# Optimization experiments

Measured on AMD Instinct MI355X. Metric: run time of the kernel, lower is better.

Reference implementation:

```python
import jax, jax.numpy as jnp
import numpy as np

L = 32            # fixed label space replacing torch.unique (labels in [0, L))
DELTA_AGG = 0.5
DELTA_DIS = 1.5
REG_W = 0.001


def safe_norm(sq):
    # sqrt with zero-safe gradient: returns 0 where sq == 0
    safe = jnp.where(sq > 0, sq, 1.0)
    return jnp.where(sq > 0, jnp.sqrt(safe), 0.0)


def _single(emb, instance, kernel, training_mask):
    D = emb.shape[0]
    tm = training_mask > 0.5
    kn = kernel > 0.5
    inst = jnp.where(tm, instance, 0).reshape(-1)          # (N,) masked instance labels
    inst_k = jnp.where(tm & kn, instance, 0).reshape(-1)   # (N,) kernel-region labels
    embf = emb.reshape(D, -1).T                            # (N, D)
    ones = jnp.ones(inst.shape, dtype=jnp.float32)

    # per-label kernel means (emb_mean), label 0 stays zero as in torch
    cnt_k = jax.ops.segment_sum(ones, inst_k, num_segments=L)            # (L,)
    sum_k = jax.ops.segment_sum(embf, inst_k, num_segments=L)            # (L, D)
    emb_mean = sum_k / jnp.maximum(cnt_k, 1.0)[:, None]
    emb_mean = emb_mean.at[0].set(0.0)

    present = cnt_k > 0
    num_instance = jnp.sum(present.astype(jnp.int32))
    nz = present & (jnp.arange(L) > 0)

    # aggregation loss: per-pixel distance to own instance's kernel mean
    diff = embf - emb_mean[inst]                                          # (N, D)
    dist = safe_norm(jnp.sum(diff * diff, axis=1))
    val = jnp.log(jax.nn.relu(dist - DELTA_AGG) ** 2 + 1.0)
    sum_v = jax.ops.segment_sum(val, inst, num_segments=L)
    cnt = jax.ops.segment_sum(ones, inst, num_segments=L)
    l_agg_per = sum_v / jnp.maximum(cnt, 1.0)
    l_agg = jnp.sum(jnp.where(nz, l_agg_per, 0.0)) / jnp.maximum(num_instance - 1, 1)

    # discrimination loss: all pairs of distinct non-background present labels
    pdiff = emb_mean[:, None, :] - emb_mean[None, :, :]                   # (L, L, D)
    pdist = safe_norm(jnp.sum(pdiff * pdiff, axis=-1))
    pval = jnp.log(jax.nn.relu(2.0 * DELTA_DIS - pdist) ** 2 + 1.0)
    pmask = nz[:, None] & nz[None, :] & ~jnp.eye(L, dtype=bool)
    n_pairs = jnp.sum(pmask.astype(jnp.float32))
    l_dis = jnp.sum(jnp.where(pmask, pval, 0.0)) / jnp.maximum(n_pairs, 1.0)
    l_dis = jnp.where(num_instance > 2, l_dis, 0.0)

    # regularizer over the num_instance present columns of emb_mean
    reg = jnp.log(safe_norm(jnp.sum(emb_mean * emb_mean, axis=1)) + 1.0)
    l_reg = jnp.sum(jnp.where(present, reg, 0.0)) / jnp.maximum(num_instance, 1) * REG_W

    loss = l_agg + l_dis + l_reg
    return jnp.where(num_instance <= 1, 0.0, loss)


def setup_inputs() -> dict:
    key = jax.random.key(0)
    k1, k2, k3, k4 = jax.random.split(key, 4)
    B, D, H, W = 8, 4, 736, 736
    emb = jax.random.normal(k1, (B, D, H, W), dtype=jnp.float32)
    instance = jax.random.randint(k2, (B, H, W), 0, L, dtype=jnp.int32)
    kernel = jax.random.uniform(k3, (B, H, W), dtype=jnp.float32)
    training_mask = jax.random.uniform(k4, (B, H, W), dtype=jnp.float32)
    return {"emb": emb, "instance": instance, "kernel": kernel, "training_mask": training_mask}


def reference(emb, instance, kernel, training_mask):
    return jax.vmap(_single)(emb, instance, kernel, training_mask)
```

## Files before the change

kernel.cpp:

```cpp
#include <hip/hip_runtime.h>

#define LBL 32
#define NPIX (736 * 736)
#define NQ (NPIX / 4)
#define NB 529
#define BATCH 8
#define DELTA_AGG 0.5f
#define DELTA_DIS 1.5f
#define REG_W 0.001f

#define CE_BASE 0
#define LAB_BASE (BATCH * NPIX * 2)
#define PA_BASE (LAB_BASE + BATCH * NPIX / 4)
#define RED_BASE (PA_BASE + BATCH * 192 * NB)
#define PC_BASE (RED_BASE + BATCH * 256)

__device__ __forceinline__ unsigned short f2bf(float f) {
  unsigned int u = __float_as_uint(f);
  unsigned int r = u + 0x7FFFu + ((u >> 16) & 1u);
  return (unsigned short)(r >> 16);
}
__device__ __forceinline__ float bfl(unsigned int w) {
  return __uint_as_float(w << 16);
}
__device__ __forceinline__ float bfh(unsigned int w) {
  return __uint_as_float(w & 0xFFFF0000u);
}

__global__ __launch_bounds__(256) void kA(
    const float* __restrict__ emb, const int* __restrict__ inst,
    const float* __restrict__ kern, const float* __restrict__ mask,
    float* __restrict__ ws) {
  const int b = blockIdx.y;
  const int t = threadIdx.x;
  __shared__ float s_cnt[LBL];
  __shared__ float s_sum[LBL * 4];
  __shared__ float s_cnta[LBL];
  if (t < LBL) { s_cnt[t] = 0.f; s_cnta[t] = 0.f; }
  if (t < LBL * 4) s_sum[t] = 0.f;
  __syncthreads();

  const long base = (long)b * NPIX;
  const int q = blockIdx.x * 256 + t;
  const int4 iv = ((const int4*)(inst + base))[q];
  const float4 kv = ((const float4*)(kern + base))[q];
  const float4 mv = ((const float4*)(mask + base))[q];
  const float* eb = emb + (long)b * 4 * NPIX;
  const float4 e0 = ((const float4*)(eb))[q];
  const float4 e1 = ((const float4*)(eb + NPIX))[q];
  const float4 e2 = ((const float4*)(eb + 2 * NPIX))[q];
  const float4 e3 = ((const float4*)(eb + 3 * NPIX))[q];

  const int labs[4] = {iv.x, iv.y, iv.z, iv.w};
  const float ks[4] = {kv.x, kv.y, kv.z, kv.w};
  const float ms[4] = {mv.x, mv.y, mv.z, mv.w};
  const float c0[4] = {e0.x, e0.y, e0.z, e0.w};
  const float c1[4] = {e1.x, e1.y, e1.z, e1.w};
  const float c2[4] = {e2.x, e2.y, e2.z, e2.w};
  const float c3[4] = {e3.x, e3.y, e3.z, e3.w};

  bool has0 = false;
  unsigned int labw = 0;
  union { unsigned short us[16]; uint4 v[2]; } pk;
#pragma unroll
  for (int j = 0; j < 4; j++) {
    const bool m = ms[j] > 0.5f;
    const int li = m ? labs[j] : 0;
    const int lk = (m && ks[j] > 0.5f) ? labs[j] : 0;
    labw |= ((unsigned int)li) << (8 * j);
    pk.us[j * 4 + 0] = f2bf(c0[j]);
    pk.us[j * 4 + 1] = f2bf(c1[j]);
    pk.us[j * 4 + 2] = f2bf(c2[j]);
    pk.us[j * 4 + 3] = f2bf(c3[j]);
    if (li > 0) atomicAdd(&s_cnta[li], 1.0f);
    if (lk > 0) {
      atomicAdd(&s_cnt[lk], 1.0f);
      atomicAdd(&s_sum[lk * 4 + 0], c0[j]);
      atomicAdd(&s_sum[lk * 4 + 1], c1[j]);
      atomicAdd(&s_sum[lk * 4 + 2], c2[j]);
      atomicAdd(&s_sum[lk * 4 + 3], c3[j]);
    } else {
      has0 = true;
    }
  }
  const size_t recq = (size_t)b * NQ + q;
  uint4* cep = (uint4*)(ws + CE_BASE);
  cep[recq * 2] = pk.v[0];
  cep[recq * 2 + 1] = pk.v[1];
  ((unsigned int*)(ws + LAB_BASE))[recq] = labw;

  if (has0) s_cnt[0] = 1.0f;
  __syncthreads();
  if (t < 192) {
    const float v = (t < 32) ? s_cnt[t] : (t < 160 ? s_sum[t - 32] : s_cnta[t - 160]);
    ws[PA_BASE + ((size_t)b * 192 + t) * NB + blockIdx.x] = v;
  }
}

__global__ __launch_bounds__(256) void kB(float* __restrict__ ws) {
  const int b = blockIdx.y;
  const int col = blockIdx.x * 4 + (threadIdx.x >> 6);
  const int lane = threadIdx.x & 63;
  const float* p = ws + PA_BASE + ((size_t)b * 192 + col) * NB;
  float s = 0.f;
  for (int g = lane; g < NB; g += 64) s += p[g];
#pragma unroll
  for (int o = 32; o > 0; o >>= 1) s += __shfl_down(s, o);
  if (lane == 0) ws[RED_BASE + b * 256 + col] = s;
}

__global__ __launch_bounds__(256) void kC(float* __restrict__ ws) {
  const int b = blockIdx.y;
  const int t = threadIdx.x;
  __shared__ float s_mean[LBL * 4];
  __shared__ float s_val[LBL];
  const float* rd = ws + RED_BASE + b * 256;
  if (t < LBL * 4) {
    const int l = t >> 2;
    s_mean[t] = (l == 0) ? 0.f : rd[32 + t] / fmaxf(rd[l], 1.0f);
  }
  if (t < LBL) s_val[t] = 0.f;
  __syncthreads();

  const int q = blockIdx.x * 256 + t;
  const size_t recq = (size_t)b * NQ + q;
  const uint4* cep = (const uint4*)(ws + CE_BASE);
  const uint4 r0 = cep[recq * 2];
  const uint4 r1 = cep[recq * 2 + 1];
  const unsigned int labw = ((const unsigned int*)(ws + LAB_BASE))[recq];

  const unsigned int wlo[4] = {r0.x, r0.z, r1.x, r1.z};
  const unsigned int whi[4] = {r0.y, r0.w, r1.y, r1.w};
#pragma unroll
  for (int j = 0; j < 4; j++) {
    const int li = (labw >> (8 * j)) & 0xFF;
    if (li > 0) {
      const float d0 = bfl(wlo[j]) - s_mean[li * 4 + 0];
      const float d1 = bfh(wlo[j]) - s_mean[li * 4 + 1];
      const float d2 = bfl(whi[j]) - s_mean[li * 4 + 2];
      const float d3 = bfh(whi[j]) - s_mean[li * 4 + 3];
      const float sq = d0 * d0 + d1 * d1 + d2 * d2 + d3 * d3;
      const float dist = (sq > 0.f) ? sqrtf(sq) : 0.f;
      const float tt = fmaxf(dist - DELTA_AGG, 0.f);
      atomicAdd(&s_val[li], logf(fmaf(tt, tt, 1.0f)));
    }
  }
  __syncthreads();
  if (t < 32) ws[PC_BASE + ((size_t)b * 32 + t) * NB + blockIdx.x] = s_val[t];
}

__global__ __launch_bounds__(1024) void kD(const float* __restrict__ ws,
                                           float* __restrict__ out) {
  const int b = blockIdx.x;
  const int t = threadIdx.x;
  const int col = t >> 5, sub = t & 31;
  const float* p = ws + PC_BASE + ((size_t)b * 32 + col) * NB;
  float s = 0.f;
  for (int g = sub; g < NB; g += 32) s += p[g];
  __shared__ float red[LBL][33];
  red[col][sub] = s;

  const float* rd = ws + RED_BASE + b * 256;
  __shared__ float sm[LBL * 4];
  __shared__ float scc[LBL];
  __shared__ float sca[LBL];
  if (t >= 512 && t < 640) {
    const int e = t - 512, l = e >> 2;
    sm[e] = (l == 0) ? 0.f : rd[32 + e] / fmaxf(rd[l], 1.0f);
  } else if (t >= 640 && t < 672) {
    scc[t - 640] = rd[t - 640];
  } else if (t >= 672 && t < 704) {
    sca[t - 672] = rd[160 + (t - 672)];
  }
  __syncthreads();
  __shared__ float sv[LBL];
  if (t < 32) {
    float v = 0.f;
#pragma unroll
    for (int k = 0; k < 32; k++) v += red[t][k];
    sv[t] = v;
  }
  __syncthreads();

  if (t < 64) {
    const int lane = t;
    const bool pres = (lane < LBL) && (scc[lane & 31] > 0.f);
    const unsigned long long bal_p = __ballot(pres);
    const int num_instance = __popcll(bal_p);
    const bool nz = pres && (lane > 0);
    const unsigned long long bal_nz = __ballot(nz);

    float agg = 0.f;
    if (nz) agg = sv[lane] / fmaxf(sca[lane], 1.0f);

    float reg = 0.f;
    if (pres) {
      float sq = 0.f;
#pragma unroll
      for (int d = 0; d < 4; d++) sq += sm[lane * 4 + d] * sm[lane * 4 + d];
      const float nrm = (sq > 0.f) ? sqrtf(sq) : 0.f;
      reg = logf(nrm + 1.0f);
    }

    float dis = 0.f, npair = 0.f;
    for (int pi = lane; pi < LBL * LBL; pi += 64) {
      const int i = pi >> 5, j = pi & 31;
      if (i != j && ((bal_nz >> i) & 1ull) && ((bal_nz >> j) & 1ull)) {
        float sq = 0.f;
#pragma unroll
        for (int d = 0; d < 4; d++) {
          const float df = sm[i * 4 + d] - sm[j * 4 + d];
          sq += df * df;
        }
        const float pdist = (sq > 0.f) ? sqrtf(sq) : 0.f;
        const float tt = fmaxf(2.0f * DELTA_DIS - pdist, 0.f);
        dis += logf(fmaf(tt, tt, 1.0f));
        npair += 1.0f;
      }
    }

#pragma unroll
    for (int o = 32; o > 0; o >>= 1) {
      agg += __shfl_down(agg, o);
      reg += __shfl_down(reg, o);
      dis += __shfl_down(dis, o);
      npair += __shfl_down(npair, o);
    }

    if (lane == 0) {
      const float l_agg = agg / fmaxf((float)(num_instance - 1), 1.0f);
      const float l_dis = (num_instance > 2) ? dis / fmaxf(npair, 1.0f) : 0.f;
      const float l_reg = reg / fmaxf((float)num_instance, 1.0f) * REG_W;
      const float loss = l_agg + l_dis + l_reg;
      out[b] = (num_instance <= 1) ? 0.f : loss;
    }
  }
}

extern "C" void kernel_launch(void* const* d_in, const int* in_sizes, int n_in,
                              void* d_out, int out_size, void* d_ws,
                              size_t ws_size, hipStream_t stream) {
  const float* emb = (const float*)d_in[0];
  const int* instance = (const int*)d_in[1];
  const float* kern = (const float*)d_in[2];
  const float* mask = (const float*)d_in[3];
  float* out = (float*)d_out;
  float* ws = (float*)d_ws;

  dim3 gridA(NB, BATCH);
  kA<<<gridA, 256, 0, stream>>>(emb, instance, kern, mask, ws);
  dim3 gridB(48, BATCH);
  kB<<<gridB, 256, 0, stream>>>(ws);
  kC<<<gridA, 256, 0, stream>>>(ws);
  kD<<<BATCH, 1024, 0, stream>>>(ws, out);
}
```

Measured before the change: 185.1 us.

## Re-read fp32 embeddings in second pass instead of stashing bf16 copies

The first pass no longer writes a bf16 copy of the embeddings. The second pass re-reads the original fp32 embeddings, leaving only the packed label word as intermediate state, and the masked-pixel count moves from the first pass to the second. Each thread now handles two quads, which halves the grid. Per-block partials are stored block-major so their writes are contiguous, and the reduction kernels are adjusted to match. This trades the bf16 write and read for a larger fp32 re-read that may be served from cache, and it removes the bf16 rounding error.

```diff
diff --git a/kernel.cpp b/kernel.cpp
--- a/kernel.cpp
+++ b/kernel.cpp
@@ -3,29 +3,17 @@
 #define LBL 32
 #define NPIX (736 * 736)
 #define NQ (NPIX / 4)
-#define NB 529
+#define QPB 512
+#define NBA 265
 #define BATCH 8
 #define DELTA_AGG 0.5f
 #define DELTA_DIS 1.5f
 #define REG_W 0.001f
 
-#define CE_BASE 0
-#define LAB_BASE (BATCH * NPIX * 2)
-#define PA_BASE (LAB_BASE + BATCH * NPIX / 4)
-#define RED_BASE (PA_BASE + BATCH * 192 * NB)
+#define LAB_BASE 0
+#define PA_BASE (BATCH * NQ)
+#define RED_BASE (PA_BASE + BATCH * NBA * 160)
 #define PC_BASE (RED_BASE + BATCH * 256)
-
-__device__ __forceinline__ unsigned short f2bf(float f) {
-  unsigned int u = __float_as_uint(f);
-  unsigned int r = u + 0x7FFFu + ((u >> 16) & 1u);
-  return (unsigned short)(r >> 16);
-}
-__device__ __forceinline__ float bfl(unsigned int w) {
-  return __uint_as_float(w << 16);
-}
-__device__ __forceinline__ float bfh(unsigned int w) {
-  return __uint_as_float(w & 0xFFFF0000u);
-}
 
 __global__ __launch_bounds__(256) void kA(
     const float* __restrict__ emb, const int* __restrict__ inst,
@@ -35,150 +23,222 @@
   const int t = threadIdx.x;
   __shared__ float s_cnt[LBL];
   __shared__ float s_sum[LBL * 4];
-  __shared__ float s_cnta[LBL];
-  if (t < LBL) { s_cnt[t] = 0.f; s_cnta[t] = 0.f; }
+  if (t < LBL) s_cnt[t] = 0.f;
   if (t < LBL * 4) s_sum[t] = 0.f;
   __syncthreads();
 
   const long base = (long)b * NPIX;
-  const int q = blockIdx.x * 256 + t;
-  const int4 iv = ((const int4*)(inst + base))[q];
-  const float4 kv = ((const float4*)(kern + base))[q];
-  const float4 mv = ((const float4*)(mask + base))[q];
   const float* eb = emb + (long)b * 4 * NPIX;
-  const float4 e0 = ((const float4*)(eb))[q];
-  const float4 e1 = ((const float4*)(eb + NPIX))[q];
-  const float4 e2 = ((const float4*)(eb + 2 * NPIX))[q];
-  const float4 e3 = ((const float4*)(eb + 3 * NPIX))[q];
-
-  const int labs[4] = {iv.x, iv.y, iv.z, iv.w};
-  const float ks[4] = {kv.x, kv.y, kv.z, kv.w};
-  const float ms[4] = {mv.x, mv.y, mv.z, mv.w};
-  const float c0[4] = {e0.x, e0.y, e0.z, e0.w};
-  const float c1[4] = {e1.x, e1.y, e1.z, e1.w};
-  const float c2[4] = {e2.x, e2.y, e2.z, e2.w};
-  const float c3[4] = {e3.x, e3.y, e3.z, e3.w};
+  const int4* ip = (const int4*)(inst + base);
+  const float4* kp = (const float4*)(kern + base);
+  const float4* mp = (const float4*)(mask + base);
+  const float4* p0 = (const float4*)(eb);
+  const float4* p1 = (const float4*)(eb + NPIX);
+  const float4* p2 = (const float4*)(eb + 2 * NPIX);
+  const float4* p3 = (const float4*)(eb + 3 * NPIX);
+
+  const int q0 = blockIdx.x * QPB + t;
+  const int q1 = q0 + 256;
+  const bool v1 = (q1 < NQ);
+
+  const int4 iva = ip[q0];
+  const float4 kva = kp[q0], mva = mp[q0];
+  const float4 ea0 = p0[q0], ea1 = p1[q0], ea2 = p2[q0], ea3 = p3[q0];
+  int4 ivb;
+  float4 kvb, mvb, eb0, eb1, eb2, eb3;
+  if (v1) {
+    ivb = ip[q1]; kvb = kp[q1]; mvb = mp[q1];
+    eb0 = p0[q1]; eb1 = p1[q1]; eb2 = p2[q1]; eb3 = p3[q1];
+  }
 
   bool has0 = false;
-  unsigned int labw = 0;
-  union { unsigned short us[16]; uint4 v[2]; } pk;
-#pragma unroll
-  for (int j = 0; j < 4; j++) {
-    const bool m = ms[j] > 0.5f;
-    const int li = m ? labs[j] : 0;
-    const int lk = (m && ks[j] > 0.5f) ? labs[j] : 0;
-    labw |= ((unsigned int)li) << (8 * j);
-    pk.us[j * 4 + 0] = f2bf(c0[j]);
-    pk.us[j * 4 + 1] = f2bf(c1[j]);
-    pk.us[j * 4 + 2] = f2bf(c2[j]);
-    pk.us[j * 4 + 3] = f2bf(c3[j]);
-    if (li > 0) atomicAdd(&s_cnta[li], 1.0f);
-    if (lk > 0) {
-      atomicAdd(&s_cnt[lk], 1.0f);
-      atomicAdd(&s_sum[lk * 4 + 0], c0[j]);
-      atomicAdd(&s_sum[lk * 4 + 1], c1[j]);
-      atomicAdd(&s_sum[lk * 4 + 2], c2[j]);
-      atomicAdd(&s_sum[lk * 4 + 3], c3[j]);
-    } else {
-      has0 = true;
-    }
-  }
-  const size_t recq = (size_t)b * NQ + q;
-  uint4* cep = (uint4*)(ws + CE_BASE);
-  cep[recq * 2] = pk.v[0];
-  cep[recq * 2 + 1] = pk.v[1];
-  ((unsigned int*)(ws + LAB_BASE))[recq] = labw;
+  unsigned int* labp = (unsigned int*)(ws + LAB_BASE) + (size_t)b * NQ;
+
+  {
+    const int labs[4] = {iva.x, iva.y, iva.z, iva.w};
+    const float ks[4] = {kva.x, kva.y, kva.z, kva.w};
+    const float ms[4] = {mva.x, mva.y, mva.z, mva.w};
+    const float c0[4] = {ea0.x, ea0.y, ea0.z, ea0.w};
+    const float c1[4] = {ea1.x, ea1.y, ea1.z, ea1.w};
+    const float c2[4] = {ea2.x, ea2.y, ea2.z, ea2.w};
+    const float c3[4] = {ea3.x, ea3.y, ea3.z, ea3.w};
+    unsigned int labw = 0;
+#pragma unroll
+    for (int j = 0; j < 4; j++) {
+      const bool m = ms[j] > 0.5f;
+      const int li = m ? labs[j] : 0;
+      const int lk = (m && ks[j] > 0.5f) ? labs[j] : 0;
+      labw |= ((unsigned int)li) << (8 * j);
+      if (lk > 0) {
+        atomicAdd(&s_cnt[lk], 1.0f);
+        atomicAdd(&s_sum[lk * 4 + 0], c0[j]);
+        atomicAdd(&s_sum[lk * 4 + 1], c1[j]);
+        atomicAdd(&s_sum[lk * 4 + 2], c2[j]);
+        atomicAdd(&s_sum[lk * 4 + 3], c3[j]);
+      } else {
+        has0 = true;
+      }
+    }
+    labp[q0] = labw;
+  }
+  if (v1) {
+    const int labs[4] = {ivb.x, ivb.y, ivb.z, ivb.w};
+    const float ks[4] = {kvb.x, kvb.y, kvb.z, kvb.w};
+    const float ms[4] = {mvb.x, mvb.y, mvb.z, mvb.w};
+    const float c0[4] = {eb0.x, eb0.y, eb0.z, eb0.w};
+    const float c1[4] = {eb1.x, eb1.y, eb1.z, eb1.w};
+    const float c2[4] = {eb2.x, eb2.y, eb2.z, eb2.w};
+    const float c3[4] = {eb3.x, eb3.y, eb3.z, eb3.w};
+    unsigned int labw = 0;
+#pragma unroll
+    for (int j = 0; j < 4; j++) {
+      const bool m = ms[j] > 0.5f;
+      const int li = m ? labs[j] : 0;
+      const int lk = (m && ks[j] > 0.5f) ? labs[j] : 0;
+      labw |= ((unsigned int)li) << (8 * j);
+      if (lk > 0) {
+        atomicAdd(&s_cnt[lk], 1.0f);
+        atomicAdd(&s_sum[lk * 4 + 0], c0[j]);
+        atomicAdd(&s_sum[lk * 4 + 1], c1[j]);
+        atomicAdd(&s_sum[lk * 4 + 2], c2[j]);
+        atomicAdd(&s_sum[lk * 4 + 3], c3[j]);
+      } else {
+        has0 = true;
+      }
+    }
+    labp[q1] = labw;
+  }
 
   if (has0) s_cnt[0] = 1.0f;
   __syncthreads();
-  if (t < 192) {
-    const float v = (t < 32) ? s_cnt[t] : (t < 160 ? s_sum[t - 32] : s_cnta[t - 160]);
-    ws[PA_BASE + ((size_t)b * 192 + t) * NB + blockIdx.x] = v;
-  }
+  float* po = ws + PA_BASE + ((size_t)b * NBA + blockIdx.x) * 160;
+  if (t < 160) po[t] = (t < 32) ? s_cnt[t] : s_sum[t - 32];
 }
 
 __global__ __launch_bounds__(256) void kB(float* __restrict__ ws) {
   const int b = blockIdx.y;
   const int col = blockIdx.x * 4 + (threadIdx.x >> 6);
   const int lane = threadIdx.x & 63;
-  const float* p = ws + PA_BASE + ((size_t)b * 192 + col) * NB;
+  const float* pa = ws + PA_BASE + (size_t)b * NBA * 160 + col;
   float s = 0.f;
-  for (int g = lane; g < NB; g += 64) s += p[g];
+  for (int g = lane; g < NBA; g += 64) s += pa[(size_t)g * 160];
 #pragma unroll
   for (int o = 32; o > 0; o >>= 1) s += __shfl_down(s, o);
   if (lane == 0) ws[RED_BASE + b * 256 + col] = s;
 }
 
-__global__ __launch_bounds__(256) void kC(float* __restrict__ ws) {
+__global__ __launch_bounds__(256) void kC(
+    const float* __restrict__ emb, float* __restrict__ ws) {
   const int b = blockIdx.y;
   const int t = threadIdx.x;
   __shared__ float s_mean[LBL * 4];
   __shared__ float s_val[LBL];
+  __shared__ float s_cta[LBL];
   const float* rd = ws + RED_BASE + b * 256;
   if (t < LBL * 4) {
     const int l = t >> 2;
     s_mean[t] = (l == 0) ? 0.f : rd[32 + t] / fmaxf(rd[l], 1.0f);
   }
-  if (t < LBL) s_val[t] = 0.f;
-  __syncthreads();
-
-  const int q = blockIdx.x * 256 + t;
-  const size_t recq = (size_t)b * NQ + q;
-  const uint4* cep = (const uint4*)(ws + CE_BASE);
-  const uint4 r0 = cep[recq * 2];
-  const uint4 r1 = cep[recq * 2 + 1];
-  const unsigned int labw = ((const unsigned int*)(ws + LAB_BASE))[recq];
-
-  const unsigned int wlo[4] = {r0.x, r0.z, r1.x, r1.z};
-  const unsigned int whi[4] = {r0.y, r0.w, r1.y, r1.w};
-#pragma unroll
-  for (int j = 0; j < 4; j++) {
-    const int li = (labw >> (8 * j)) & 0xFF;
-    if (li > 0) {
-      const float d0 = bfl(wlo[j]) - s_mean[li * 4 + 0];
-      const float d1 = bfh(wlo[j]) - s_mean[li * 4 + 1];
-      const float d2 = bfl(whi[j]) - s_mean[li * 4 + 2];
-      const float d3 = bfh(whi[j]) - s_mean[li * 4 + 3];
-      const float sq = d0 * d0 + d1 * d1 + d2 * d2 + d3 * d3;
-      const float dist = (sq > 0.f) ? sqrtf(sq) : 0.f;
-      const float tt = fmaxf(dist - DELTA_AGG, 0.f);
-      atomicAdd(&s_val[li], logf(fmaf(tt, tt, 1.0f)));
-    }
-  }
-  __syncthreads();
-  if (t < 32) ws[PC_BASE + ((size_t)b * 32 + t) * NB + blockIdx.x] = s_val[t];
+  if (t < LBL) {
+    s_val[t] = 0.f;
+    s_cta[t] = 0.f;
+  }
+  __syncthreads();
+
+  const float* ebase = emb + (long)b * 4 * NPIX;
+  const float4* p0 = (const float4*)(ebase);
+  const float4* p1 = (const float4*)(ebase + NPIX);
+  const float4* p2 = (const float4*)(ebase + 2 * NPIX);
+  const float4* p3 = (const float4*)(ebase + 3 * NPIX);
+  const unsigned int* labp = (const unsigned int*)(ws + LAB_BASE) + (size_t)b * NQ;
+
+  const int q0 = blockIdx.x * QPB + t;
+  const int q1 = q0 + 256;
+  const bool v1 = (q1 < NQ);
+
+  const unsigned int lwa = labp[q0];
+  const float4 ea0 = p0[q0], ea1 = p1[q0], ea2 = p2[q0], ea3 = p3[q0];
+  unsigned int lwb = 0;
+  float4 eb0, eb1, eb2, eb3;
+  if (v1) {
+    lwb = labp[q1];
+    eb0 = p0[q1]; eb1 = p1[q1]; eb2 = p2[q1]; eb3 = p3[q1];
+  }
+
+  {
+    const float c0[4] = {ea0.x, ea0.y, ea0.z, ea0.w};
+    const float c1[4] = {ea1.x, ea1.y, ea1.z, ea1.w};
+    const float c2[4] = {ea2.x, ea2.y, ea2.z, ea2.w};
+    const float c3[4] = {ea3.x, ea3.y, ea3.z, ea3.w};
+#pragma unroll
+    for (int j = 0; j < 4; j++) {
+      const int li = (lwa >> (8 * j)) & 0xFF;
+      if (li > 0) {
+        const float d0 = c0[j] - s_mean[li * 4 + 0];
+        const float d1 = c1[j] - s_mean[li * 4 + 1];
+        const float d2 = c2[j] - s_mean[li * 4 + 2];
+        const float d3 = c3[j] - s_mean[li * 4 + 3];
+        const float sq = d0 * d0 + d1 * d1 + d2 * d2 + d3 * d3;
+        const float dist = (sq > 0.f) ? sqrtf(sq) : 0.f;
+        const float tt = fmaxf(dist - DELTA_AGG, 0.f);
+        atomicAdd(&s_val[li], logf(fmaf(tt, tt, 1.0f)));
+        atomicAdd(&s_cta[li], 1.0f);
+      }
+    }
+  }
+  if (v1) {
+    const float c0[4] = {eb0.x, eb0.y, eb0.z, eb0.w};
+    const float c1[4] = {eb1.x, eb1.y, eb1.z, eb1.w};
+    const float c2[4] = {eb2.x, eb2.y, eb2.z, eb2.w};
+    const float c3[4] = {eb3.x, eb3.y, eb3.z, eb3.w};
+#pragma unroll
+    for (int j = 0; j < 4; j++) {
+      const int li = (lwb >> (8 * j)) & 0xFF;
+      if (li > 0) {
+        const float d0 = c0[j] - s_mean[li * 4 + 0];
+        const float d1 = c1[j] - s_mean[li * 4 + 1];
+        const float d2 = c2[j] - s_mean[li * 4 + 2];
+        const float d3 = c3[j] - s_mean[li * 4 + 3];
+        const float sq = d0 * d0 + d1 * d1 + d2 * d2 + d3 * d3;
+        const float dist = (sq > 0.f) ? sqrtf(sq) : 0.f;
+        const float tt = fmaxf(dist - DELTA_AGG, 0.f);
+        atomicAdd(&s_val[li], logf(fmaf(tt, tt, 1.0f)));
+        atomicAdd(&s_cta[li], 1.0f);
+      }
+    }
+  }
+  __syncthreads();
+  float* po = ws + PC_BASE + ((size_t)b * NBA + blockIdx.x) * 64;
+  if (t < 64) po[t] = (t < 32) ? s_val[t] : s_cta[t - 32];
 }
 
 __global__ __launch_bounds__(1024) void kD(const float* __restrict__ ws,
                                            float* __restrict__ out) {
   const int b = blockIdx.x;
   const int t = threadIdx.x;
-  const int col = t >> 5, sub = t & 31;
-  const float* p = ws + PC_BASE + ((size_t)b * 32 + col) * NB;
+  const int col = t >> 4, sub = t & 15;
+  const float* pc = ws + PC_BASE + (size_t)b * NBA * 64 + col;
   float s = 0.f;
-  for (int g = sub; g < NB; g += 32) s += p[g];
-  __shared__ float red[LBL][33];
+  for (int g = sub; g < NBA; g += 16) s += pc[(size_t)g * 64];
+  __shared__ float red[64][17];
   red[col][sub] = s;
 
   const float* rd = ws + RED_BASE + b * 256;
   __shared__ float sm[LBL * 4];
   __shared__ float scc[LBL];
-  __shared__ float sca[LBL];
   if (t >= 512 && t < 640) {
     const int e = t - 512, l = e >> 2;
     sm[e] = (l == 0) ? 0.f : rd[32 + e] / fmaxf(rd[l], 1.0f);
   } else if (t >= 640 && t < 672) {
     scc[t - 640] = rd[t - 640];
-  } else if (t >= 672 && t < 704) {
-    sca[t - 672] = rd[160 + (t - 672)];
-  }
-  __syncthreads();
-  __shared__ float sv[LBL];
-  if (t < 32) {
+  }
+  __syncthreads();
+  __shared__ float svca[64];
+  if (t < 64) {
     float v = 0.f;
 #pragma unroll
-    for (int k = 0; k < 32; k++) v += red[t][k];
-    sv[t] = v;
+    for (int k = 0; k < 16; k++) v += red[t][k];
+    svca[t] = v;
   }
   __syncthreads();
 
@@ -191,7 +251,7 @@
     const unsigned long long bal_nz = __ballot(nz);
 
     float agg = 0.f;
-    if (nz) agg = sv[lane] / fmaxf(sca[lane], 1.0f);
+    if (nz) agg = svca[lane] / fmaxf(svca[32 + lane], 1.0f);
 
     float reg = 0.f;
     if (pres) {
@@ -247,10 +307,10 @@
   float* out = (float*)d_out;
   float* ws = (float*)d_ws;
 
-  dim3 gridA(NB, BATCH);
+  dim3 gridA(NBA, BATCH);
   kA<<<gridA, 256, 0, stream>>>(emb, instance, kern, mask, ws);
-  dim3 gridB(48, BATCH);
+  dim3 gridB(40, BATCH);
   kB<<<gridB, 256, 0, stream>>>(ws);
-  kC<<<gridA, 256, 0, stream>>>(ws);
+  kC<<<gridA, 256, 0, stream>>>(emb, ws);
   kD<<<BATCH, 1024, 0, stream>>>(ws, out);
 }
```

Result: slower. 196.1 us (+6.0%).

## Fuse four passes into one cooperative kernel keeping packed embeddings in LDS

Applied to the files above, without the earlier changes.

Replaces the four separate kernels with one cooperative kernel using three grid-wide syncs. Each block handles a fixed chunk of pixels and keeps the bf16-packed embeddings and labels in shared memory between the kernel-mean pass and the aggregation pass. This removes the global workspace write and re-read of packed embeddings and several launches. In exchange it needs large LDS per block, a grid size capped by co-residency, grid barriers, and single-block serial reductions.

```diff
diff --git a/kernel.cpp b/kernel.cpp
--- a/kernel.cpp
+++ b/kernel.cpp
@@ -1,24 +1,26 @@
 #include <hip/hip_runtime.h>
+#include <hip/hip_cooperative_groups.h>
+
+namespace cg = cooperative_groups;
 
 #define LBL 32
 #define NPIX (736 * 736)
 #define NQ (NPIX / 4)
-#define NB 529
+#define GPB 128
+#define QPB (NQ / GPB)
 #define BATCH 8
 #define DELTA_AGG 0.5f
 #define DELTA_DIS 1.5f
 #define REG_W 0.001f
 
-#define CE_BASE 0
-#define LAB_BASE (BATCH * NPIX * 2)
-#define PA_BASE (LAB_BASE + BATCH * NPIX / 4)
-#define RED_BASE (PA_BASE + BATCH * 192 * NB)
-#define PC_BASE (RED_BASE + BATCH * 256)
-
-__device__ __forceinline__ unsigned short f2bf(float f) {
+#define PA_BASE 0
+#define RED_BASE (BATCH * GPB * 192)
+#define PV_BASE (RED_BASE + BATCH * 256)
+
+__device__ __forceinline__ unsigned int f2bf(float f) {
   unsigned int u = __float_as_uint(f);
   unsigned int r = u + 0x7FFFu + ((u >> 16) & 1u);
-  return (unsigned short)(r >> 16);
+  return r >> 16;
 }
 __device__ __forceinline__ float bfl(unsigned int w) {
   return __uint_as_float(w << 16);
@@ -27,93 +29,97 @@
   return __uint_as_float(w & 0xFFFF0000u);
 }
 
-__global__ __launch_bounds__(256) void kA(
+__global__ __launch_bounds__(256, 4) void kFused(
     const float* __restrict__ emb, const int* __restrict__ inst,
     const float* __restrict__ kern, const float* __restrict__ mask,
-    float* __restrict__ ws) {
+    float* __restrict__ ws, float* __restrict__ out) {
   const int b = blockIdx.y;
+  const int g = blockIdx.x;
   const int t = threadIdx.x;
+
+  __shared__ unsigned int eL[8][QPB];
+  __shared__ unsigned int labL[QPB];
   __shared__ float s_cnt[LBL];
   __shared__ float s_sum[LBL * 4];
-  __shared__ float s_cnta[LBL];
-  if (t < LBL) { s_cnt[t] = 0.f; s_cnta[t] = 0.f; }
+  __shared__ float s_cta[LBL];
+  __shared__ float s_val[LBL];
+  __shared__ float s_mean[LBL * 4];
+  __shared__ float red4[128];
+  __shared__ float sv[LBL];
+
+  if (t < LBL) { s_cnt[t] = 0.f; s_cta[t] = 0.f; }
   if (t < LBL * 4) s_sum[t] = 0.f;
   __syncthreads();
 
   const long base = (long)b * NPIX;
-  const int q = blockIdx.x * 256 + t;
-  const int4 iv = ((const int4*)(inst + base))[q];
-  const float4 kv = ((const float4*)(kern + base))[q];
-  const float4 mv = ((const float4*)(mask + base))[q];
-  const float* eb = emb + (long)b * 4 * NPIX;
-  const float4 e0 = ((const float4*)(eb))[q];
-  const float4 e1 = ((const float4*)(eb + NPIX))[q];
-  const float4 e2 = ((const float4*)(eb + 2 * NPIX))[q];
-  const float4 e3 = ((const float4*)(eb + 3 * NPIX))[q];
-
-  const int labs[4] = {iv.x, iv.y, iv.z, iv.w};
-  const float ks[4] = {kv.x, kv.y, kv.z, kv.w};
-  const float ms[4] = {mv.x, mv.y, mv.z, mv.w};
-  const float c0[4] = {e0.x, e0.y, e0.z, e0.w};
-  const float c1[4] = {e1.x, e1.y, e1.z, e1.w};
-  const float c2[4] = {e2.x, e2.y, e2.z, e2.w};
-  const float c3[4] = {e3.x, e3.y, e3.z, e3.w};
-
+  const float* ebase = emb + (long)b * 4 * NPIX;
+  const int4* ip = (const int4*)(inst + base);
+  const float4* kp = (const float4*)(kern + base);
+  const float4* mp = (const float4*)(mask + base);
+  const float4* p0 = (const float4*)(ebase);
+  const float4* p1 = (const float4*)(ebase + NPIX);
+  const float4* p2 = (const float4*)(ebase + 2 * NPIX);
+  const float4* p3 = (const float4*)(ebase + 3 * NPIX);
+
+  const int qStart = g * QPB;
   bool has0 = false;
-  unsigned int labw = 0;
-  union { unsigned short us[16]; uint4 v[2]; } pk;
-#pragma unroll
-  for (int j = 0; j < 4; j++) {
-    const bool m = ms[j] > 0.5f;
-    const int li = m ? labs[j] : 0;
-    const int lk = (m && ks[j] > 0.5f) ? labs[j] : 0;
-    labw |= ((unsigned int)li) << (8 * j);
-    pk.us[j * 4 + 0] = f2bf(c0[j]);
-    pk.us[j * 4 + 1] = f2bf(c1[j]);
-    pk.us[j * 4 + 2] = f2bf(c2[j]);
-    pk.us[j * 4 + 3] = f2bf(c3[j]);
-    if (li > 0) atomicAdd(&s_cnta[li], 1.0f);
-    if (lk > 0) {
-      atomicAdd(&s_cnt[lk], 1.0f);
-      atomicAdd(&s_sum[lk * 4 + 0], c0[j]);
-      atomicAdd(&s_sum[lk * 4 + 1], c1[j]);
-      atomicAdd(&s_sum[lk * 4 + 2], c2[j]);
-      atomicAdd(&s_sum[lk * 4 + 3], c3[j]);
-    } else {
-      has0 = true;
-    }
-  }
-  const size_t recq = (size_t)b * NQ + q;
-  uint4* cep = (uint4*)(ws + CE_BASE);
-  cep[recq * 2] = pk.v[0];
-  cep[recq * 2 + 1] = pk.v[1];
-  ((unsigned int*)(ws + LAB_BASE))[recq] = labw;
-
+
+  for (int r = 0; r < 5; ++r) {
+    const int qb = r * 256 + t;
+    if (qb >= QPB) break;
+    const int qg = qStart + qb;
+    const int4 iv = ip[qg];
+    const float4 kv = kp[qg];
+    const float4 mv = mp[qg];
+    const float4 e0 = p0[qg], e1 = p1[qg], e2 = p2[qg], e3 = p3[qg];
+
+    const int labs[4] = {iv.x, iv.y, iv.z, iv.w};
+    const float ks[4] = {kv.x, kv.y, kv.z, kv.w};
+    const float ms[4] = {mv.x, mv.y, mv.z, mv.w};
+    const float c0[4] = {e0.x, e0.y, e0.z, e0.w};
+    const float c1[4] = {e1.x, e1.y, e1.z, e1.w};
+    const float c2[4] = {e2.x, e2.y, e2.z, e2.w};
+    const float c3[4] = {e3.x, e3.y, e3.z, e3.w};
+
+    unsigned int labw = 0;
+#pragma unroll
+    for (int j = 0; j < 4; j++) {
+      const bool m = ms[j] > 0.5f;
+      const int li = m ? labs[j] : 0;
+      const int lk = (m && ks[j] > 0.5f) ? labs[j] : 0;
+      labw |= ((unsigned int)li) << (8 * j);
+      eL[j * 2 + 0][qb] = f2bf(c0[j]) | (f2bf(c1[j]) << 16);
+      eL[j * 2 + 1][qb] = f2bf(c2[j]) | (f2bf(c3[j]) << 16);
+      if (li > 0) atomicAdd(&s_cta[li], 1.0f);
+      if (lk > 0) {
+        atomicAdd(&s_cnt[lk], 1.0f);
+        atomicAdd(&s_sum[lk * 4 + 0], c0[j]);
+        atomicAdd(&s_sum[lk * 4 + 1], c1[j]);
+        atomicAdd(&s_sum[lk * 4 + 2], c2[j]);
+        atomicAdd(&s_sum[lk * 4 + 3], c3[j]);
+      } else {
+        has0 = true;
+      }
+    }
+    labL[qb] = labw;
+  }
   if (has0) s_cnt[0] = 1.0f;
   __syncthreads();
-  if (t < 192) {
-    const float v = (t < 32) ? s_cnt[t] : (t < 160 ? s_sum[t - 32] : s_cnta[t - 160]);
-    ws[PA_BASE + ((size_t)b * 192 + t) * NB + blockIdx.x] = v;
-  }
-}
-
-__global__ __launch_bounds__(256) void kB(float* __restrict__ ws) {
-  const int b = blockIdx.y;
-  const int col = blockIdx.x * 4 + (threadIdx.x >> 6);
-  const int lane = threadIdx.x & 63;
-  const float* p = ws + PA_BASE + ((size_t)b * 192 + col) * NB;
-  float s = 0.f;
-  for (int g = lane; g < NB; g += 64) s += p[g];
-#pragma unroll
-  for (int o = 32; o > 0; o >>= 1) s += __shfl_down(s, o);
-  if (lane == 0) ws[RED_BASE + b * 256 + col] = s;
-}
-
-__global__ __launch_bounds__(256) void kC(float* __restrict__ ws) {
-  const int b = blockIdx.y;
-  const int t = threadIdx.x;
-  __shared__ float s_mean[LBL * 4];
-  __shared__ float s_val[LBL];
+  {
+    float* po = ws + PA_BASE + ((size_t)(b * GPB + g)) * 192;
+    if (t < 192)
+      po[t] = (t < 32) ? s_cnt[t] : (t < 160 ? s_sum[t - 32] : s_cta[t - 160]);
+  }
+  cg::this_grid().sync();
+
+  if (g == 0 && t < 192) {
+    const float* pa = ws + PA_BASE + (size_t)b * GPB * 192 + t;
+    float s = 0.f;
+    for (int k = 0; k < GPB; k++) s += pa[(size_t)k * 192];
+    ws[RED_BASE + b * 256 + t] = s;
+  }
+  cg::this_grid().sync();
+
   const float* rd = ws + RED_BASE + b * 256;
   if (t < LBL * 4) {
     const int l = t >> 2;
@@ -122,82 +128,63 @@
   if (t < LBL) s_val[t] = 0.f;
   __syncthreads();
 
-  const int q = blockIdx.x * 256 + t;
-  const size_t recq = (size_t)b * NQ + q;
-  const uint4* cep = (const uint4*)(ws + CE_BASE);
-  const uint4 r0 = cep[recq * 2];
-  const uint4 r1 = cep[recq * 2 + 1];
-  const unsigned int labw = ((const unsigned int*)(ws + LAB_BASE))[recq];
-
-  const unsigned int wlo[4] = {r0.x, r0.z, r1.x, r1.z};
-  const unsigned int whi[4] = {r0.y, r0.w, r1.y, r1.w};
-#pragma unroll
-  for (int j = 0; j < 4; j++) {
-    const int li = (labw >> (8 * j)) & 0xFF;
-    if (li > 0) {
-      const float d0 = bfl(wlo[j]) - s_mean[li * 4 + 0];
-      const float d1 = bfh(wlo[j]) - s_mean[li * 4 + 1];
-      const float d2 = bfl(whi[j]) - s_mean[li * 4 + 2];
-      const float d3 = bfh(whi[j]) - s_mean[li * 4 + 3];
-      const float sq = d0 * d0 + d1 * d1 + d2 * d2 + d3 * d3;
-      const float dist = (sq > 0.f) ? sqrtf(sq) : 0.f;
-      const float tt = fmaxf(dist - DELTA_AGG, 0.f);
-      atomicAdd(&s_val[li], logf(fmaf(tt, tt, 1.0f)));
-    }
-  }
-  __syncthreads();
-  if (t < 32) ws[PC_BASE + ((size_t)b * 32 + t) * NB + blockIdx.x] = s_val[t];
-}
-
-__global__ __launch_bounds__(1024) void kD(const float* __restrict__ ws,
-                                           float* __restrict__ out) {
-  const int b = blockIdx.x;
-  const int t = threadIdx.x;
-  const int col = t >> 5, sub = t & 31;
-  const float* p = ws + PC_BASE + ((size_t)b * 32 + col) * NB;
-  float s = 0.f;
-  for (int g = sub; g < NB; g += 32) s += p[g];
-  __shared__ float red[LBL][33];
-  red[col][sub] = s;
-
-  const float* rd = ws + RED_BASE + b * 256;
-  __shared__ float sm[LBL * 4];
-  __shared__ float scc[LBL];
-  __shared__ float sca[LBL];
-  if (t >= 512 && t < 640) {
-    const int e = t - 512, l = e >> 2;
-    sm[e] = (l == 0) ? 0.f : rd[32 + e] / fmaxf(rd[l], 1.0f);
-  } else if (t >= 640 && t < 672) {
-    scc[t - 640] = rd[t - 640];
-  } else if (t >= 672 && t < 704) {
-    sca[t - 672] = rd[160 + (t - 672)];
-  }
-  __syncthreads();
-  __shared__ float sv[LBL];
-  if (t < 32) {
-    float v = 0.f;
-#pragma unroll
-    for (int k = 0; k < 32; k++) v += red[t][k];
-    sv[t] = v;
-  }
-  __syncthreads();
+  for (int r = 0; r < 5; ++r) {
+    const int qb = r * 256 + t;
+    if (qb >= QPB) break;
+    const unsigned int labw = labL[qb];
+#pragma unroll
+    for (int j = 0; j < 4; j++) {
+      const int li = (labw >> (8 * j)) & 0xFF;
+      if (li > 0) {
+        const unsigned int w0 = eL[j * 2 + 0][qb];
+        const unsigned int w1 = eL[j * 2 + 1][qb];
+        const float d0 = bfl(w0) - s_mean[li * 4 + 0];
+        const float d1 = bfh(w0) - s_mean[li * 4 + 1];
+        const float d2 = bfl(w1) - s_mean[li * 4 + 2];
+        const float d3 = bfh(w1) - s_mean[li * 4 + 3];
+        const float sq = d0 * d0 + d1 * d1 + d2 * d2 + d3 * d3;
+        const float dist = (sq > 0.f) ? sqrtf(sq) : 0.f;
+        const float tt = fmaxf(dist - DELTA_AGG, 0.f);
+        atomicAdd(&s_val[li], logf(fmaf(tt, tt, 1.0f)));
+      }
+    }
+  }
+  __syncthreads();
+  if (t < 32) ws[PV_BASE + ((size_t)(b * GPB + g)) * 32 + t] = s_val[t];
+  cg::this_grid().sync();
+
+  if (g != 0) return;
+  {
+    const float* pv = ws + PV_BASE + (size_t)b * GPB * 32;
+    if (t < 128) {
+      const int c = t >> 5, col = t & 31;
+      float s = 0.f;
+      for (int k = c; k < GPB; k += 4) s += pv[(size_t)k * 32 + col];
+      red4[t] = s;
+    }
+    __syncthreads();
+    if (t < 32) sv[t] = red4[t] + red4[32 + t] + red4[64 + t] + red4[96 + t];
+    __syncthreads();
+  }
 
   if (t < 64) {
     const int lane = t;
-    const bool pres = (lane < LBL) && (scc[lane & 31] > 0.f);
+    const float cntk = (lane < LBL) ? rd[lane] : 0.f;
+    const float cnta = (lane < LBL) ? rd[160 + lane] : 0.f;
+    const bool pres = (lane < LBL) && (cntk > 0.f);
     const unsigned long long bal_p = __ballot(pres);
     const int num_instance = __popcll(bal_p);
     const bool nz = pres && (lane > 0);
     const unsigned long long bal_nz = __ballot(nz);
 
     float agg = 0.f;
-    if (nz) agg = sv[lane] / fmaxf(sca[lane], 1.0f);
+    if (nz) agg = sv[lane] / fmaxf(cnta, 1.0f);
 
     float reg = 0.f;
     if (pres) {
       float sq = 0.f;
 #pragma unroll
-      for (int d = 0; d < 4; d++) sq += sm[lane * 4 + d] * sm[lane * 4 + d];
+      for (int d = 0; d < 4; d++) sq += s_mean[lane * 4 + d] * s_mean[lane * 4 + d];
       const float nrm = (sq > 0.f) ? sqrtf(sq) : 0.f;
       reg = logf(nrm + 1.0f);
     }
@@ -209,7 +196,7 @@
         float sq = 0.f;
 #pragma unroll
         for (int d = 0; d < 4; d++) {
-          const float df = sm[i * 4 + d] - sm[j * 4 + d];
+          const float df = s_mean[i * 4 + d] - s_mean[j * 4 + d];
           sq += df * df;
         }
         const float pdist = (sq > 0.f) ? sqrtf(sq) : 0.f;
@@ -247,10 +234,8 @@
   float* out = (float*)d_out;
   float* ws = (float*)d_ws;
 
-  dim3 gridA(NB, BATCH);
-  kA<<<gridA, 256, 0, stream>>>(emb, instance, kern, mask, ws);
-  dim3 gridB(48, BATCH);
-  kB<<<gridB, 256, 0, stream>>>(ws);
-  kC<<<gridA, 256, 0, stream>>>(ws);
-  kD<<<BATCH, 1024, 0, stream>>>(ws, out);
-}
+  void* args[] = {(void*)&emb, (void*)&instance, (void*)&kern,
+                  (void*)&mask, (void*)&ws, (void*)&out};
+  hipLaunchCooperativeKernel(kFused, dim3(GPB, BATCH), dim3(256), args, 0,
+                             stream);
+}
```

Result: slower. 509.2 us (+175.2%).
